# Optimization experiments

Measured on AMD Instinct MI355X. Metric: run time of the kernel, lower is better.

The kernel has to match this reference:

```python
import jax, jax.numpy as jnp
import numpy as np

B, T, DM, H, DK, DV = 2, 2048, 1024, 16, 64, 64


def setup_inputs() -> dict:
    key = jax.random.key(0)
    k = jax.random.split(key, 7)
    std_k = np.float32(1.0 / np.sqrt(DK))
    std_v = np.float32(1.0 / np.sqrt(DV))
    return {
        "xq": jax.random.normal(k[0], (B, T, DM), jnp.float32),
        "xk": jax.random.normal(k[1], (B, T, DM), jnp.float32),
        "xv": jax.random.normal(k[2], (B, T, DM), jnp.float32),
        "mask": jnp.ones((B, T), jnp.float32),  # padding mask: 1 = keep
        "w_q": jax.random.normal(k[3], (H, DM, DK), jnp.float32) * std_k,
        "w_k": jax.random.normal(k[4], (H, DM, DK), jnp.float32) * std_k,
        "w_v": jax.random.normal(k[5], (H, DM, DV), jnp.float32) * std_v,
        "w_o": jax.random.normal(k[6], (H * DV, DM), jnp.float32) * np.float32(1.0 / np.sqrt(H * DV)),
        "b_o": jnp.zeros((DM,), jnp.float32),
    }


def reference(xq, xk, xv, mask, w_q, w_k, w_v, w_o, b_o):
    d_k = w_q.shape[-1]
    # per-head projections: [B,T,DM] x [H,DM,DK] -> [B,H,T,DK]
    q = jnp.einsum('bsd,hdk->bhsk', xq, w_q)
    kk = jnp.einsum('btd,hdk->bhtk', xk, w_k)
    v = jnp.einsum('btd,hdv->bhtv', xv, w_v)
    # NOTE: source divides by d_k (not sqrt(d_k)) -- kept faithful
    scores = jnp.einsum('bhsk,bhtk->bhst', q, kk) / jnp.float32(d_k)
    # _padding_mask: multiply by mask broadcast over key dim, then any exact
    # zero (masked OR coincidentally zero score) becomes -inf -- kept faithful
    masked = scores * mask[:, None, None, :]
    scores = jnp.where(masked == 0.0, -jnp.inf, masked)
    attn = jax.nn.softmax(scores, axis=-1)
    out = jnp.einsum('bhst,bhtv->bhsv', attn, v)  # [B,H,T,DV]
    b, h, t, dv = out.shape
    concat = out.transpose(0, 2, 1, 3).reshape(b, t, h * dv)
    return concat @ w_o + b_o
```

## Files before the change

kernel.cpp:

```cpp
#include <hip/hip_runtime.h>
#include <hip/hip_bf16.h>


typedef __attribute__((ext_vector_type(8))) short short8;
typedef __attribute__((ext_vector_type(4))) short short4v;
typedef __attribute__((ext_vector_type(4))) float f32x4;
typedef __attribute__((ext_vector_type(4))) int i32x4;

__device__ __forceinline__ short f2bf(float f) {
  union { float f; unsigned u; } v; v.f = f;
  unsigned r = v.u + 0x7FFFu + ((v.u >> 16) & 1u);
  return (short)(r >> 16);
}

#define GLD_LDS(g, l) __builtin_amdgcn_global_load_lds( \
    (const __attribute__((address_space(1))) void*)(g), \
    (__attribute__((address_space(3))) void*)(l), 16, 0, 0)

__global__ __launch_bounds__(256) void prep_w(
    const float* __restrict__ wq, const float* __restrict__ wk,
    const float* __restrict__ wv, const float* __restrict__ wo,
    short* __restrict__ Wall, short* __restrict__ Wot)
{
  const int bx = blockIdx.x, tid = threadIdx.x;
  __shared__ float Lt[64][65];
  if (bx < 768) {
    int z = bx >> 8, inner = bx & 255;
    const float* w = z == 0 ? wq : (z == 1 ? wk : wv);
    short* Wt = Wall + (size_t)z * 1048576;
    int h = inner >> 4, d0 = (inner & 15) * 64;
#pragma unroll
    for (int it = 0; it < 4; it++) {
      int e = tid + it * 256;
      int dl = e >> 4, k4 = (e & 15) * 4;
      f32x4 v = *(const f32x4*)(w + ((size_t)(h * 1024 + d0 + dl) * 64) + k4);
#pragma unroll
      for (int j = 0; j < 4; j++) Lt[dl][k4 + j] = v[j];
    }
    __syncthreads();
#pragma unroll
    for (int it = 0; it < 4; it++) {
      int e = tid + it * 256;
      int kl = e >> 4, dq = e & 15;
      short4v s;
#pragma unroll
      for (int j = 0; j < 4; j++) s[j] = f2bf(Lt[dq * 4 + j][kl]);
      *(short4v*)(Wt + (size_t)(h * 64 + kl) * 1024 + d0 + dq * 4) = s;
    }
  } else {
    int bz = bx - 768;
    int k0 = (bz >> 4) * 64, n0 = (bz & 15) * 64;
#pragma unroll
    for (int it = 0; it < 4; it++) {
      int e = tid + it * 256;
      int kl = e >> 4, n4 = (e & 15) * 4;
      f32x4 v = *(const f32x4*)(wo + (size_t)(k0 + kl) * 1024 + n0 + n4);
#pragma unroll
      for (int j = 0; j < 4; j++) Lt[kl][n4 + j] = v[j];
    }
    __syncthreads();
#pragma unroll
    for (int it = 0; it < 4; it++) {
      int e = tid + it * 256;
      int nl = e >> 4, kq = e & 15;
      short4v s;
#pragma unroll
      for (int j = 0; j < 4; j++) s[j] = f2bf(Lt[kq * 4 + j][nl]);
      *(short4v*)(Wot + (size_t)(n0 + nl) * 1024 + k0 + kq * 4) = s;
    }
  }
}

__global__ __launch_bounds__(256) void proj_qkv4(
    const float* __restrict__ xq, const float* __restrict__ xk,
    const float* __restrict__ xv, const short* __restrict__ Wall,
    short* __restrict__ Qb, short* __restrict__ Kt2, short* __restrict__ Vt2)
{
  const int z = blockIdx.z;
  const float* X  = z == 0 ? xq : (z == 1 ? xk : xv);
  const short* Wt = Wall + (size_t)z * 1048576;

  const int t0 = blockIdx.x * 128;
  const int n0 = blockIdx.y * 128;
  const int tid = threadIdx.x, w = tid >> 6, lane = tid & 63;
  const int c = lane & 15, q4 = lane >> 4;
  const int wn = (w & 1) * 64, wt = (w >> 1) * 64;
  const int srow = lane >> 2, scol = (lane & 3) * 8;

  __shared__ __align__(16) short Al[2][2][4096];
  __shared__ __align__(16) short Bl[2][2][4096];

  f32x4 acc[4][4] = {};
  f32x4 xr[2][2][2];

#define PSTAGE_A(BUF, K0) do { \
    _Pragma("unroll") \
    for (int sub = 0; sub < 2; sub++) { \
      _Pragma("unroll") \
      for (int i = 0; i < 2; i++) { \
        int rg = (w * 2 + i) * 16; \
        GLD_LDS(Wt + (size_t)(n0 + rg + srow) * 1024 + (K0) + sub * 32 + scol, &Al[BUF][sub][rg * 32]); \
      } \
    } \
  } while (0)

#define XLOAD(K0) do { \
    _Pragma("unroll") \
    for (int i = 0; i < 2; i++) { \
      _Pragma("unroll") \
      for (int sub = 0; sub < 2; sub++) { \
        const float* xs = X + (size_t)(t0 + (w * 2 + i) * 16 + srow) * 1024 + (K0) + sub * 32 + scol; \
        xr[i][sub][0] = *(const f32x4*)(xs); \
        xr[i][sub][1] = *(const f32x4*)(xs + 4); \
      } \
    } \
  } while (0)

#define XWRITE(BUF) do { \
    _Pragma("unroll") \
    for (int i = 0; i < 2; i++) { \
      _Pragma("unroll") \
      for (int sub = 0; sub < 2; sub++) { \
        unsigned p0, p1, p2, p3; \
        asm("v_cvt_pk_bf16_f32 %0, %1, %2" : "=v"(p0) : "v"(xr[i][sub][0][0]), "v"(xr[i][sub][0][1])); \
        asm("v_cvt_pk_bf16_f32 %0, %1, %2" : "=v"(p1) : "v"(xr[i][sub][0][2]), "v"(xr[i][sub][0][3])); \
        asm("v_cvt_pk_bf16_f32 %0, %1, %2" : "=v"(p2) : "v"(xr[i][sub][1][0]), "v"(xr[i][sub][1][1])); \
        asm("v_cvt_pk_bf16_f32 %0, %1, %2" : "=v"(p3) : "v"(xr[i][sub][1][2]), "v"(xr[i][sub][1][3])); \
        union { i32x4 iv; short8 s; } pk; \
        pk.iv[0] = (int)p0; pk.iv[1] = (int)p1; pk.iv[2] = (int)p2; pk.iv[3] = (int)p3; \
        *(short8*)(&Bl[BUF][sub][((w * 2 + i) * 16 + srow) * 32 + scol]) = pk.s; \
      } \
    } \
  } while (0)

#define PCOMP(BUF) do { \
    _Pragma("unroll") \
    for (int sub = 0; sub < 2; sub++) { \
      short8 a[4], bfr[4]; \
      if (z != 2) { \
        _Pragma("unroll") \
        for (int i = 0; i < 4; i++) \
          a[i] = *(const short8*)(&Al[BUF][sub][(wn + i * 16 + c) * 32 + q4 * 8]); \
        _Pragma("unroll") \
        for (int j = 0; j < 4; j++) \
          bfr[j] = *(const short8*)(&Bl[BUF][sub][(wt + j * 16 + c) * 32 + q4 * 8]); \
      } else { \
        _Pragma("unroll") \
        for (int i = 0; i < 4; i++) \
          a[i] = *(const short8*)(&Bl[BUF][sub][(wt + i * 16 + c) * 32 + q4 * 8]); \
        _Pragma("unroll") \
        for (int j = 0; j < 4; j++) \
          bfr[j] = *(const short8*)(&Al[BUF][sub][(wn + j * 16 + c) * 32 + q4 * 8]); \
      } \
      _Pragma("unroll") \
      for (int i = 0; i < 4; i++) \
        _Pragma("unroll") \
        for (int j = 0; j < 4; j++) \
          acc[i][j] = __builtin_amdgcn_mfma_f32_16x16x32_bf16(a[i], bfr[j], acc[i][j], 0, 0, 0); \
    } \
  } while (0)

  PSTAGE_A(0, 0);
  XLOAD(0);
  XWRITE(0);
  asm volatile("s_waitcnt vmcnt(0)" ::: "memory");
  __syncthreads();
  int cur = 0;
  for (int p = 0; p < 15; ++p) {
    PSTAGE_A(cur ^ 1, (p + 1) * 64);
    XLOAD((p + 1) * 64);
    PCOMP(cur);
    XWRITE(cur ^ 1);
    asm volatile("s_waitcnt vmcnt(0)" ::: "memory");
    __syncthreads();
    cur ^= 1;
  }
  PCOMP(cur);
#undef PSTAGE_A
#undef XLOAD
#undef XWRITE
#undef PCOMP

  if (z != 2) {
#pragma unroll
    for (int i = 0; i < 4; i++)
#pragma unroll
      for (int j = 0; j < 4; j++) {
        int n = n0 + wn + i * 16 + q4 * 4;
        int trow = t0 + wt + j * 16 + c;
        int b = trow >> 11, t = trow & 2047;
        int h = n >> 6, cc = n & 63;
        int bh = b * 16 + h;
        f32x4 v = acc[i][j];
        short4v pk;
#pragma unroll
        for (int r = 0; r < 4; r++) pk[r] = f2bf(v[r]);
        if (z == 0) {
          *(short4v*)(Qb + (size_t)(bh * 2048 + t) * 64 + cc) = pk;
        } else {
          int t5 = t & 31, s_ = t5 >> 4, c_ = t5 & 15;
          size_t base = (size_t)bh * 131072 + (t >> 5) * 2048;
          size_t off = base + ((s_ * 2 + (cc >> 5)) * 16 + c_) * 32 +
                       ((cc >> 3) & 3) * 8 + (cc & 7);
          *(short4v*)(Kt2 + off) = pk;
        }
      }
  } else {
#pragma unroll
    for (int i = 0; i < 4; i++)
#pragma unroll
      for (int j = 0; j < 4; j++) {
        int tq = t0 + wt + i * 16 + q4 * 4;
        int n = n0 + wn + j * 16 + c;
        int b = tq >> 11, t = tq & 2047;
        int h = n >> 6, cc = n & 63;
        int bh = b * 16 + h;
        int t5 = t & 31;
        int kpb = ((t5 >> 2) & 3) * 8 + ((t5 >> 4) & 1) * 4;
        size_t base = (size_t)bh * 131072 + (t >> 5) * 2048;
        f32x4 v = acc[i][j];
        short4v pk;
#pragma unroll
        for (int r = 0; r < 4; r++) pk[r] = f2bf(v[r]);
        *(short4v*)(Vt2 + base + (size_t)cc * 32 + kpb) = pk;
      }
  }
}

__global__ __launch_bounds__(256, 2) void attn14(
    const short* __restrict__ Qb, const short* __restrict__ Kt2,
    const short* __restrict__ Vt2, const float* __restrict__ mask,
    short* __restrict__ AO)
{
  const int bh = blockIdx.x;
  const int tblk = blockIdx.y;
  const int b = bh >> 4, h = bh & 15;
  const short* Qh = Qb  + (size_t)bh * 131072;
  const short* Kh = Kt2 + (size_t)bh * 131072;
  const short* Vh = Vt2 + (size_t)bh * 131072;

  const int tid = threadIdx.x, w = tid >> 6, lane = tid & 63;
  const int c = lane & 15, q4 = lane >> 4;
  const int qrow0 = tblk * 128 + w * 32;

  __shared__ __align__(16) short KV2[2][8192];
  __shared__ __align__(16) float cmL[2048];
  __shared__ __align__(16) float cbL[2048];

  const int ch = c * 4 + q4;
  const int rdo = (ch ^ ((ch >> 3) & 3)) * 8;
  const int sch = (lane ^ ((lane >> 3) & 3)) * 8;

  {
    const float LOG2E_64c = 1.44269504088896f * 0.015625f;
    f32x4 m0 = *(const f32x4*)(mask + b * 2048 + tid * 8);
    f32x4 m1 = *(const f32x4*)(mask + b * 2048 + tid * 8 + 4);
    *(f32x4*)(&cmL[tid * 8])     = m0 * LOG2E_64c;
    *(f32x4*)(&cmL[tid * 8 + 4]) = m1 * LOG2E_64c;
    *(f32x4*)(&cbL[tid * 8])     = (m0 - 1.0f) * 240.0f;
    *(f32x4*)(&cbL[tid * 8 + 4]) = (m1 - 1.0f) * 240.0f;
  }

  short8 qa[2][2];
#pragma unroll
  for (int u = 0; u < 2; u++)
#pragma unroll
    for (int dc = 0; dc < 2; dc++)
      qa[u][dc] = *(const short8*)(Qh + (size_t)(qrow0 + u * 16 + c) * 64 + dc * 32 + q4 * 8);

  f32x4 acc[2][4] = {};
  float l[2] = {0.f, 0.f};

  const int g0 = w * 2;

#define STAGE(BI, P) do { \
    const short* s0 = (g0 < 4) ? (Kh + (size_t)(2 * (P)) * 2048 + g0 * 512) \
                               : (Vh + (size_t)(2 * (P)) * 2048 + (g0 - 4) * 512); \
    GLD_LDS(s0 + sch,         &KV2[BI][g0 * 512]); \
    GLD_LDS(s0 + 512 + sch,   &KV2[BI][g0 * 512 + 512]); \
    const short* s1 = (g0 < 4) ? (Kh + (size_t)(2 * (P) + 1) * 2048 + g0 * 512) \
                               : (Vh + (size_t)(2 * (P) + 1) * 2048 + (g0 - 4) * 512); \
    GLD_LDS(s1 + sch,         &KV2[BI][4096 + g0 * 512]); \
    GLD_LDS(s1 + 512 + sch,   &KV2[BI][4096 + g0 * 512 + 512]); \
  } while (0)

#define BODY1(KB, TT) do { \
    const short* Kb = (KB); \
    short8 kf[2][2], va[4]; \
    _Pragma("unroll") \
    for (int s = 0; s < 2; s++) \
      _Pragma("unroll") \
      for (int dc = 0; dc < 2; dc++) \
        kf[s][dc] = *(const short8*)(Kb + (s * 2 + dc) * 512 + rdo); \
    _Pragma("unroll") \
    for (int vs = 0; vs < 4; vs++) \
      va[vs] = *(const short8*)(Kb + 2048 + vs * 512 + rdo); \
    f32x4 st[2][2]; \
    _Pragma("unroll") \
    for (int u = 0; u < 2; u++) \
      _Pragma("unroll") \
      for (int s = 0; s < 2; s++) { \
        f32x4 z = {}; \
        z = __builtin_amdgcn_mfma_f32_16x16x32_bf16(kf[s][0], qa[u][0], z, 0, 0, 0); \
        st[u][s] = __builtin_amdgcn_mfma_f32_16x16x32_bf16(kf[s][1], qa[u][1], z, 0, 0, 0); \
      } \
    f32x4 cm[2], cb[2]; \
    _Pragma("unroll") \
    for (int s = 0; s < 2; s++) { \
      cm[s] = *(const f32x4*)(&cmL[(TT) * 32 + q4 * 4 + s * 16]); \
      cb[s] = *(const f32x4*)(&cbL[(TT) * 32 + q4 * 4 + s * 16]); \
    } \
    _Pragma("unroll") \
    for (int u = 0; u < 2; u++) { \
      unsigned pkd[2][2]; \
      _Pragma("unroll") \
      for (int s = 0; s < 2; s++) { \
        float e0 = __builtin_amdgcn_exp2f(st[u][s][0] * cm[s][0] + cb[s][0]); \
        float e1 = __builtin_amdgcn_exp2f(st[u][s][1] * cm[s][1] + cb[s][1]); \
        float e2 = __builtin_amdgcn_exp2f(st[u][s][2] * cm[s][2] + cb[s][2]); \
        float e3 = __builtin_amdgcn_exp2f(st[u][s][3] * cm[s][3] + cb[s][3]); \
        l[u] += (e0 + e1) + (e2 + e3); \
        unsigned p01, p23; \
        asm("v_cvt_pk_bf16_f32 %0, %1, %2" : "=v"(p01) : "v"(e0), "v"(e1)); \
        asm("v_cvt_pk_bf16_f32 %0, %1, %2" : "=v"(p23) : "v"(e2), "v"(e3)); \
        pkd[s][0] = p01; pkd[s][1] = p23; \
      } \
      union { i32x4 i; short8 s; } pb; \
      pb.i[0] = (int)pkd[0][0]; pb.i[1] = (int)pkd[0][1]; \
      pb.i[2] = (int)pkd[1][0]; pb.i[3] = (int)pkd[1][1]; \
      _Pragma("unroll") \
      for (int vs = 0; vs < 4; vs++) \
        acc[u][vs] = __builtin_amdgcn_mfma_f32_16x16x32_bf16(va[vs], pb.s, acc[u][vs], 0, 0, 0); \
    } \
  } while (0)

#define BODY(BI, P) do { \
    BODY1(&KV2[BI][0],    2 * (P)); \
    BODY1(&KV2[BI][4096], 2 * (P) + 1); \
  } while (0)

  __syncthreads();
  asm volatile("s_waitcnt vmcnt(0)" ::: "memory");
  STAGE(0, 0);
  asm volatile("s_waitcnt vmcnt(0)" ::: "memory");
  __syncthreads();
  int cur = 0;
  for (int p = 0; p < 31; ++p) {
    STAGE(cur ^ 1, p + 1);
    BODY(cur, p);
    asm volatile("s_waitcnt vmcnt(0)" ::: "memory");
    __syncthreads();
    cur ^= 1;
  }
  BODY(cur, 31);
#undef STAGE
#undef BODY1
#undef BODY

#pragma unroll
  for (int u = 0; u < 2; u++) {
    float lu = l[u];
    lu += __shfl_xor(lu, 16);
    lu += __shfl_xor(lu, 32);
    float inv = 1.0f / lu;
    size_t row = (size_t)b * 2048 + qrow0 + u * 16 + c;
#pragma unroll
    for (int vs = 0; vs < 4; vs++) {
      f32x4 v = acc[u][vs];
      short4v pk;
#pragma unroll
      for (int r = 0; r < 4; r++) pk[r] = f2bf(v[r] * inv);
      *(short4v*)(AO + row * 1024 + h * 64 + vs * 16 + q4 * 4) = pk;
    }
  }
}

__global__ __launch_bounds__(256) void out_proj3(
    const short* __restrict__ AO, const short* __restrict__ Wot,
    const float* __restrict__ bo, float* __restrict__ out)
{
  const int t0 = blockIdx.x * 128;
  const int n0 = blockIdx.y * 128;
  const int tid = threadIdx.x, w = tid >> 6, lane = tid & 63;
  const int c = lane & 15, q4 = lane >> 4;
  const int wn = (w & 1) * 64, wt = (w >> 1) * 64;
  const int srow = lane >> 2, scol = (lane & 3) * 8;

  __shared__ __align__(16) short Al[2][2][4096];
  __shared__ __align__(16) short Bl[2][2][4096];

  f32x4 acc[4][4] = {};

#define PSTAGE(BUF, K0) do { \
    _Pragma("unroll") \
    for (int sub = 0; sub < 2; sub++) { \
      _Pragma("unroll") \
      for (int i = 0; i < 2; i++) { \
        int rg = (w * 2 + i) * 16; \
        GLD_LDS(Wot + (size_t)(n0 + rg + srow) * 1024 + (K0) + sub * 32 + scol, &Al[BUF][sub][rg * 32]); \
        GLD_LDS(AO  + (size_t)(t0 + rg + srow) * 1024 + (K0) + sub * 32 + scol, &Bl[BUF][sub][rg * 32]); \
      } \
    } \
  } while (0)

#define PCOMP(BUF) do { \
    _Pragma("unroll") \
    for (int sub = 0; sub < 2; sub++) { \
      short8 a[4], bfr[4]; \
      _Pragma("unroll") \
      for (int i = 0; i < 4; i++) \
        a[i] = *(const short8*)(&Al[BUF][sub][(wn + i * 16 + c) * 32 + q4 * 8]); \
      _Pragma("unroll") \
      for (int j = 0; j < 4; j++) \
        bfr[j] = *(const short8*)(&Bl[BUF][sub][(wt + j * 16 + c) * 32 + q4 * 8]); \
      _Pragma("unroll") \
      for (int i = 0; i < 4; i++) \
        _Pragma("unroll") \
        for (int j = 0; j < 4; j++) \
          acc[i][j] = __builtin_amdgcn_mfma_f32_16x16x32_bf16(a[i], bfr[j], acc[i][j], 0, 0, 0); \
    } \
  } while (0)

  PSTAGE(0, 0);
  asm volatile("s_waitcnt vmcnt(0)" ::: "memory");
  __syncthreads();
  int cur = 0;
  for (int p = 0; p < 15; ++p) {
    PSTAGE(cur ^ 1, (p + 1) * 64);
    PCOMP(cur);
    asm volatile("s_waitcnt vmcnt(0)" ::: "memory");
    __syncthreads();
    cur ^= 1;
  }
  PCOMP(cur);
#undef PSTAGE
#undef PCOMP

#pragma unroll
  for (int i = 0; i < 4; i++)
#pragma unroll
    for (int j = 0; j < 4; j++) {
      int n = n0 + wn + i * 16 + q4 * 4;
      int trow = t0 + wt + j * 16 + c;
      f32x4 v = acc[i][j] + *(const f32x4*)(bo + n);
      *(f32x4*)(out + (size_t)trow * 1024 + n) = v;
    }
}

extern "C" void kernel_launch(void* const* d_in, const int* in_sizes, int n_in,
                              void* d_out, int out_size, void* d_ws, size_t ws_size,
                              hipStream_t stream)
{
  (void)in_sizes; (void)n_in; (void)out_size; (void)ws_size;
  const float* xq   = (const float*)d_in[0];
  const float* xk   = (const float*)d_in[1];
  const float* xv   = (const float*)d_in[2];
  const float* mask = (const float*)d_in[3];
  const float* wq   = (const float*)d_in[4];
  const float* wk   = (const float*)d_in[5];
  const float* wv   = (const float*)d_in[6];
  const float* wo   = (const float*)d_in[7];
  const float* bo   = (const float*)d_in[8];
  float* out = (float*)d_out;

  char* ws = (char*)d_ws;
  short* Wall = (short*)(ws + (size_t)0);
  short* Wot  = (short*)(ws + ((size_t)6 << 20));
  short* AO   = (short*)(ws + ((size_t)8 << 20));
  short* Qb   = (short*)(ws + ((size_t)16 << 20));
  short* Kt2  = (short*)(ws + ((size_t)24 << 20));
  short* Vt2  = (short*)(ws + ((size_t)32 << 20));

  prep_w<<<1024, 256, 0, stream>>>(wq, wk, wv, wo, Wall, Wot);
  proj_qkv4<<<dim3(32, 8, 3), 256, 0, stream>>>(xq, xk, xv, Wall, Qb, Kt2, Vt2);
  attn14<<<dim3(32, 16), 256, 0, stream>>>(Qb, Kt2, Vt2, mask, AO);
  out_proj3<<<dim3(32, 8), 256, 0, stream>>>(AO, Wot, bo, out);
}
```

Baseline: 239.8 us.

## Load X operands directly into MFMA registers; halve out-projection row tile

The QKV projection stops staging the converted X tile through shared memory. Each lane now loads the fp32 activations it needs for its MFMA fragments straight from global memory, converts them to bf16 in registers, and prefetches the next K-step during compute. This removes the LDS writes and reads for X, at the cost of more register pressure and some redundant global reads, because the two waves sharing a row range both load the same X rows. The output projection tile shrinks from 128 to 64 rows to launch twice as many blocks and improve occupancy. Workspace offsets for Q, K and V are also moved.

```diff
diff --git a/kernel.cpp b/kernel.cpp
--- a/kernel.cpp
+++ b/kernel.cpp
@@ -71,7 +71,7 @@
   }
 }
 
-__global__ __launch_bounds__(256) void proj_qkv4(
+__global__ __launch_bounds__(256) void proj_qkv5(
     const float* __restrict__ xq, const float* __restrict__ xk,
     const float* __restrict__ xv, const short* __restrict__ Wall,
     short* __restrict__ Qb, short* __restrict__ Kt2, short* __restrict__ Vt2)
@@ -88,10 +88,9 @@
   const int srow = lane >> 2, scol = (lane & 3) * 8;
 
   __shared__ __align__(16) short Al[2][2][4096];
-  __shared__ __align__(16) short Bl[2][2][4096];
 
   f32x4 acc[4][4] = {};
-  f32x4 xr[2][2][2];
+  f32x4 xr[2][4][2];
 
 #define PSTAGE_A(BUF, K0) do { \
     _Pragma("unroll") \
@@ -106,79 +105,70 @@
 
 #define XLOAD(K0) do { \
     _Pragma("unroll") \
-    for (int i = 0; i < 2; i++) { \
-      _Pragma("unroll") \
-      for (int sub = 0; sub < 2; sub++) { \
-        const float* xs = X + (size_t)(t0 + (w * 2 + i) * 16 + srow) * 1024 + (K0) + sub * 32 + scol; \
-        xr[i][sub][0] = *(const f32x4*)(xs); \
-        xr[i][sub][1] = *(const f32x4*)(xs + 4); \
-      } \
-    } \
-  } while (0)
-
-#define XWRITE(BUF) do { \
-    _Pragma("unroll") \
-    for (int i = 0; i < 2; i++) { \
-      _Pragma("unroll") \
-      for (int sub = 0; sub < 2; sub++) { \
+    for (int sub = 0; sub < 2; sub++) { \
+      _Pragma("unroll") \
+      for (int f = 0; f < 4; f++) { \
+        const float* xs = X + (size_t)(t0 + wt + f * 16 + c) * 1024 + (K0) + sub * 32 + q4 * 8; \
+        xr[sub][f][0] = *(const f32x4*)(xs); \
+        xr[sub][f][1] = *(const f32x4*)(xs + 4); \
+      } \
+    } \
+  } while (0)
+
+#define PCOMP(BUF, NK) do { \
+    short8 xb[2][4]; \
+    _Pragma("unroll") \
+    for (int sub = 0; sub < 2; sub++) { \
+      _Pragma("unroll") \
+      for (int f = 0; f < 4; f++) { \
         unsigned p0, p1, p2, p3; \
-        asm("v_cvt_pk_bf16_f32 %0, %1, %2" : "=v"(p0) : "v"(xr[i][sub][0][0]), "v"(xr[i][sub][0][1])); \
-        asm("v_cvt_pk_bf16_f32 %0, %1, %2" : "=v"(p1) : "v"(xr[i][sub][0][2]), "v"(xr[i][sub][0][3])); \
-        asm("v_cvt_pk_bf16_f32 %0, %1, %2" : "=v"(p2) : "v"(xr[i][sub][1][0]), "v"(xr[i][sub][1][1])); \
-        asm("v_cvt_pk_bf16_f32 %0, %1, %2" : "=v"(p3) : "v"(xr[i][sub][1][2]), "v"(xr[i][sub][1][3])); \
+        asm("v_cvt_pk_bf16_f32 %0, %1, %2" : "=v"(p0) : "v"(xr[sub][f][0][0]), "v"(xr[sub][f][0][1])); \
+        asm("v_cvt_pk_bf16_f32 %0, %1, %2" : "=v"(p1) : "v"(xr[sub][f][0][2]), "v"(xr[sub][f][0][3])); \
+        asm("v_cvt_pk_bf16_f32 %0, %1, %2" : "=v"(p2) : "v"(xr[sub][f][1][0]), "v"(xr[sub][f][1][1])); \
+        asm("v_cvt_pk_bf16_f32 %0, %1, %2" : "=v"(p3) : "v"(xr[sub][f][1][2]), "v"(xr[sub][f][1][3])); \
         union { i32x4 iv; short8 s; } pk; \
         pk.iv[0] = (int)p0; pk.iv[1] = (int)p1; pk.iv[2] = (int)p2; pk.iv[3] = (int)p3; \
-        *(short8*)(&Bl[BUF][sub][((w * 2 + i) * 16 + srow) * 32 + scol]) = pk.s; \
-      } \
-    } \
-  } while (0)
-
-#define PCOMP(BUF) do { \
-    _Pragma("unroll") \
-    for (int sub = 0; sub < 2; sub++) { \
-      short8 a[4], bfr[4]; \
+        xb[sub][f] = pk.s; \
+      } \
+    } \
+    XLOAD(NK);                          \
+    _Pragma("unroll") \
+    for (int sub = 0; sub < 2; sub++) { \
+      short8 wf[4]; \
+      _Pragma("unroll") \
+      for (int i = 0; i < 4; i++) \
+        wf[i] = *(const short8*)(&Al[BUF][sub][(wn + i * 16 + c) * 32 + q4 * 8]); \
       if (z != 2) { \
         _Pragma("unroll") \
         for (int i = 0; i < 4; i++) \
-          a[i] = *(const short8*)(&Al[BUF][sub][(wn + i * 16 + c) * 32 + q4 * 8]); \
-        _Pragma("unroll") \
-        for (int j = 0; j < 4; j++) \
-          bfr[j] = *(const short8*)(&Bl[BUF][sub][(wt + j * 16 + c) * 32 + q4 * 8]); \
+          _Pragma("unroll") \
+          for (int j = 0; j < 4; j++) \
+            acc[i][j] = __builtin_amdgcn_mfma_f32_16x16x32_bf16(wf[i], xb[sub][j], acc[i][j], 0, 0, 0); \
       } else { \
         _Pragma("unroll") \
         for (int i = 0; i < 4; i++) \
-          a[i] = *(const short8*)(&Bl[BUF][sub][(wt + i * 16 + c) * 32 + q4 * 8]); \
-        _Pragma("unroll") \
-        for (int j = 0; j < 4; j++) \
-          bfr[j] = *(const short8*)(&Al[BUF][sub][(wn + j * 16 + c) * 32 + q4 * 8]); \
-      } \
-      _Pragma("unroll") \
-      for (int i = 0; i < 4; i++) \
-        _Pragma("unroll") \
-        for (int j = 0; j < 4; j++) \
-          acc[i][j] = __builtin_amdgcn_mfma_f32_16x16x32_bf16(a[i], bfr[j], acc[i][j], 0, 0, 0); \
-    } \
-  } while (0)
-
+          _Pragma("unroll") \
+          for (int j = 0; j < 4; j++) \
+            acc[i][j] = __builtin_amdgcn_mfma_f32_16x16x32_bf16(xb[sub][i], wf[j], acc[i][j], 0, 0, 0); \
+      } \
+    } \
+  } while (0)
+
+  XLOAD(0);
   PSTAGE_A(0, 0);
-  XLOAD(0);
-  XWRITE(0);
   asm volatile("s_waitcnt vmcnt(0)" ::: "memory");
   __syncthreads();
   int cur = 0;
   for (int p = 0; p < 15; ++p) {
     PSTAGE_A(cur ^ 1, (p + 1) * 64);
-    XLOAD((p + 1) * 64);
-    PCOMP(cur);
-    XWRITE(cur ^ 1);
+    PCOMP(cur, (p + 1) * 64);
     asm volatile("s_waitcnt vmcnt(0)" ::: "memory");
     __syncthreads();
     cur ^= 1;
   }
-  PCOMP(cur);
+  PCOMP(cur, 0);
 #undef PSTAGE_A
 #undef XLOAD
-#undef XWRITE
 #undef PCOMP
 
   if (z != 2) {
@@ -375,21 +365,21 @@
   }
 }
 
-__global__ __launch_bounds__(256) void out_proj3(
+__global__ __launch_bounds__(256) void out_proj4(
     const short* __restrict__ AO, const short* __restrict__ Wot,
     const float* __restrict__ bo, float* __restrict__ out)
 {
-  const int t0 = blockIdx.x * 128;
+  const int t0 = blockIdx.x * 64;
   const int n0 = blockIdx.y * 128;
   const int tid = threadIdx.x, w = tid >> 6, lane = tid & 63;
   const int c = lane & 15, q4 = lane >> 4;
-  const int wn = (w & 1) * 64, wt = (w >> 1) * 64;
+  const int wn = (w & 1) * 64, wt = (w >> 1) * 32;
   const int srow = lane >> 2, scol = (lane & 3) * 8;
 
   __shared__ __align__(16) short Al[2][2][4096];
-  __shared__ __align__(16) short Bl[2][2][4096];
-
-  f32x4 acc[4][4] = {};
+  __shared__ __align__(16) short Bl[2][2][2048];
+
+  f32x4 acc[4][2] = {};
 
 #define PSTAGE(BUF, K0) do { \
     _Pragma("unroll") \
@@ -398,25 +388,26 @@
       for (int i = 0; i < 2; i++) { \
         int rg = (w * 2 + i) * 16; \
         GLD_LDS(Wot + (size_t)(n0 + rg + srow) * 1024 + (K0) + sub * 32 + scol, &Al[BUF][sub][rg * 32]); \
-        GLD_LDS(AO  + (size_t)(t0 + rg + srow) * 1024 + (K0) + sub * 32 + scol, &Bl[BUF][sub][rg * 32]); \
-      } \
+      } \
+      int rb = w * 16; \
+      GLD_LDS(AO + (size_t)(t0 + rb + srow) * 1024 + (K0) + sub * 32 + scol, &Bl[BUF][sub][rb * 32]); \
     } \
   } while (0)
 
 #define PCOMP(BUF) do { \
     _Pragma("unroll") \
     for (int sub = 0; sub < 2; sub++) { \
-      short8 a[4], bfr[4]; \
+      short8 a[4], bfr[2]; \
       _Pragma("unroll") \
       for (int i = 0; i < 4; i++) \
         a[i] = *(const short8*)(&Al[BUF][sub][(wn + i * 16 + c) * 32 + q4 * 8]); \
       _Pragma("unroll") \
-      for (int j = 0; j < 4; j++) \
+      for (int j = 0; j < 2; j++) \
         bfr[j] = *(const short8*)(&Bl[BUF][sub][(wt + j * 16 + c) * 32 + q4 * 8]); \
       _Pragma("unroll") \
       for (int i = 0; i < 4; i++) \
         _Pragma("unroll") \
-        for (int j = 0; j < 4; j++) \
+        for (int j = 0; j < 2; j++) \
           acc[i][j] = __builtin_amdgcn_mfma_f32_16x16x32_bf16(a[i], bfr[j], acc[i][j], 0, 0, 0); \
     } \
   } while (0)
@@ -439,7 +430,7 @@
 #pragma unroll
   for (int i = 0; i < 4; i++)
 #pragma unroll
-    for (int j = 0; j < 4; j++) {
+    for (int j = 0; j < 2; j++) {
       int n = n0 + wn + i * 16 + q4 * 4;
       int trow = t0 + wt + j * 16 + c;
       f32x4 v = acc[i][j] + *(const f32x4*)(bo + n);
@@ -467,12 +458,12 @@
   short* Wall = (short*)(ws + (size_t)0);
   short* Wot  = (short*)(ws + ((size_t)6 << 20));
   short* AO   = (short*)(ws + ((size_t)8 << 20));
-  short* Qb   = (short*)(ws + ((size_t)16 << 20));
-  short* Kt2  = (short*)(ws + ((size_t)24 << 20));
-  short* Vt2  = (short*)(ws + ((size_t)32 << 20));
+  short* Qb   = (short*)(ws + ((size_t)32 << 20));
+  short* Kt2  = (short*)(ws + ((size_t)40 << 20));
+  short* Vt2  = (short*)(ws + ((size_t)48 << 20));
 
   prep_w<<<1024, 256, 0, stream>>>(wq, wk, wv, wo, Wall, Wot);
-  proj_qkv4<<<dim3(32, 8, 3), 256, 0, stream>>>(xq, xk, xv, Wall, Qb, Kt2, Vt2);
+  proj_qkv5<<<dim3(32, 8, 3), 256, 0, stream>>>(xq, xk, xv, Wall, Qb, Kt2, Vt2);
   attn14<<<dim3(32, 16), 256, 0, stream>>>(Qb, Kt2, Vt2, mask, AO);
-  out_proj3<<<dim3(32, 8), 256, 0, stream>>>(AO, Wot, bo, out);
-}
+  out_proj4<<<dim3(64, 8), 256, 0, stream>>>(AO, Wot, bo, out);
+}
```

After: 277.2 us. +15.6%, slower.
